# Kernel tuning notes

Hardware: AMD Instinct MI355X
Metric: run time of the kernel (lower is better)

The kernel has to match this reference:

```python
import jax, jax.numpy as jnp
import numpy as np

VOCAB = 50257
SMALL = 512
LARGE = 1024
B, S = 4, 2048


def setup_inputs() -> dict:
    key = jax.random.key(0)
    k1, k2, k3, k4 = jax.random.split(key, 4)
    input_ids = jax.random.randint(k1, (B, S), 0, VOCAB)
    weight = jax.random.normal(k2, (VOCAB, SMALL), dtype=jnp.float32) * 0.02
    # coeffs_weight stored as (large-small, small); init like normalized uniform
    cw = jax.random.uniform(k3, (LARGE - SMALL, SMALL), dtype=jnp.float32)
    coeffs_weight = cw / jnp.sum(cw, axis=-1, keepdims=True)
    residual_weight = jax.random.uniform(k4, (VOCAB, LARGE), dtype=jnp.float32,
                                         minval=-0.01, maxval=0.01)
    return {"input_ids": input_ids, "weight": weight,
            "coeffs_weight": coeffs_weight, "residual_weight": residual_weight}


def reference(input_ids, weight, coeffs_weight, residual_weight):
    # get_params(): expand width then add residual over the FULL vocab
    # expanded part: weight @ coeffs_weight.T -> (vocab, large-small)
    expanded = jnp.matmul(weight, coeffs_weight.T)
    full = jnp.concatenate([weight, expanded], axis=1) + residual_weight  # (vocab, large)
    # F.embedding gather
    return jnp.take(full, input_ids, axis=0)  # (B, S, large)
```

## Files before the change

### kernel.cpp

```cpp
#include <hip/hip_runtime.h>
#include <hip/hip_bf16.h>

typedef __attribute__((ext_vector_type(8))) short bf16x8;
typedef __attribute__((ext_vector_type(4))) float f32x4;

constexpr int VOCAB = 50257;
constexpr int SMALL = 512;
constexpr int LARGE = 1024;
constexpr int NTOK  = 4 * 2048;

static __device__ __forceinline__ unsigned short f2bf(float f) {
    __hip_bfloat16 h = __float2bfloat16(f);
    return *reinterpret_cast<unsigned short*>(&h);
}

__global__ __launch_bounds__(256) void k_gather(const int* __restrict__ ids,
                                                const float* __restrict__ weight,
                                                const float* __restrict__ residual,
                                                float* __restrict__ out,
                                                unsigned short* __restrict__ a_bf16) {
    int i  = blockIdx.x * 256 + threadIdx.x;
    int t  = i >> 7;
    int c  = (i & 127) << 2;
    int id = ids[t];
    const float4 w = *reinterpret_cast<const float4*>(weight   + (size_t)id * SMALL + c);
    const float4 r = *reinterpret_cast<const float4*>(residual + (size_t)id * LARGE + c);
    float4 o;
    o.x = w.x + r.x; o.y = w.y + r.y; o.z = w.z + r.z; o.w = w.w + r.w;
    *reinterpret_cast<float4*>(out + (size_t)t * LARGE + c) = o;
    ushort4 a;
    a.x = f2bf(w.x); a.y = f2bf(w.y); a.z = f2bf(w.z); a.w = f2bf(w.w);
    *reinterpret_cast<ushort4*>(a_bf16 + (size_t)t * SMALL + c) = a;
}

__global__ __launch_bounds__(256) void k_cvt_coeffs(const float* __restrict__ coeffs,
                                                    unsigned short* __restrict__ b_bf16) {
    int i = blockIdx.x * 256 + threadIdx.x;
    int e = i << 2;
    const float4 cvec = *reinterpret_cast<const float4*>(coeffs + e);
    ushort4 b;
    b.x = f2bf(cvec.x); b.y = f2bf(cvec.y); b.z = f2bf(cvec.z); b.w = f2bf(cvec.w);
    *reinterpret_cast<ushort4*>(b_bf16 + e) = b;
}

__global__ __launch_bounds__(256) void k_gemm(const int* __restrict__ ids,
                                              const unsigned short* __restrict__ A,
                                              const unsigned short* __restrict__ B,
                                              const float* __restrict__ residual,
                                              float* __restrict__ out) {
    const int wid  = threadIdx.x >> 6;
    const int lane = threadIdx.x & 63;
    const int bm   = blockIdx.x >> 3;
    const int bn   = blockIdx.x & 7;
    const int row0 = bm * 128 + wid * 32;
    const int col0 = bn * 64;
    const int lr   = lane & 15;
    const int lk   = (lane >> 4) * 8;

    f32x4 acc[2][4] = {};

    const unsigned short* pa0 = A + (size_t)(row0 + lr) * SMALL + lk;
    const unsigned short* pa1 = A + (size_t)(row0 + 16 + lr) * SMALL + lk;
    const unsigned short* pb  = B + (size_t)(col0 + lr) * SMALL + lk;

    for (int k0 = 0; k0 < 512; k0 += 32) {
        bf16x8 a0 = *reinterpret_cast<const bf16x8*>(pa0 + k0);
        bf16x8 a1 = *reinterpret_cast<const bf16x8*>(pa1 + k0);
        bf16x8 b0 = *reinterpret_cast<const bf16x8*>(pb + k0);
        bf16x8 b1 = *reinterpret_cast<const bf16x8*>(pb + 16 * SMALL + k0);
        bf16x8 b2 = *reinterpret_cast<const bf16x8*>(pb + 32 * SMALL + k0);
        bf16x8 b3 = *reinterpret_cast<const bf16x8*>(pb + 48 * SMALL + k0);
        acc[0][0] = __builtin_amdgcn_mfma_f32_16x16x32_bf16(a0, b0, acc[0][0], 0, 0, 0);
        acc[0][1] = __builtin_amdgcn_mfma_f32_16x16x32_bf16(a0, b1, acc[0][1], 0, 0, 0);
        acc[0][2] = __builtin_amdgcn_mfma_f32_16x16x32_bf16(a0, b2, acc[0][2], 0, 0, 0);
        acc[0][3] = __builtin_amdgcn_mfma_f32_16x16x32_bf16(a0, b3, acc[0][3], 0, 0, 0);
        acc[1][0] = __builtin_amdgcn_mfma_f32_16x16x32_bf16(a1, b0, acc[1][0], 0, 0, 0);
        acc[1][1] = __builtin_amdgcn_mfma_f32_16x16x32_bf16(a1, b1, acc[1][1], 0, 0, 0);
        acc[1][2] = __builtin_amdgcn_mfma_f32_16x16x32_bf16(a1, b2, acc[1][2], 0, 0, 0);
        acc[1][3] = __builtin_amdgcn_mfma_f32_16x16x32_bf16(a1, b3, acc[1][3], 0, 0, 0);
    }

    const int rbase = row0 + (lane >> 4) * 4;
    const int cbase = SMALL + col0 + lr;
#pragma unroll
    for (int m = 0; m < 2; ++m) {
#pragma unroll
        for (int r = 0; r < 4; ++r) {
            const int row = rbase + m * 16 + r;
            const int id  = ids[row];
            const float* res = residual + (size_t)id * LARGE + cbase;
            float*       op  = out      + (size_t)row * LARGE + cbase;
#pragma unroll
            for (int n = 0; n < 4; ++n)
                op[n * 16] = acc[m][n][r] + res[n * 16];
        }
    }
}

extern "C" void kernel_launch(void* const* d_in, const int* in_sizes, int n_in,
                              void* d_out, int out_size, void* d_ws, size_t ws_size,
                              hipStream_t stream) {
    const int*   ids      = (const int*)d_in[0];
    const float* weight   = (const float*)d_in[1];
    const float* coeffs   = (const float*)d_in[2];
    const float* residual = (const float*)d_in[3];
    float*       out      = (float*)d_out;

    unsigned short* a_bf16 = (unsigned short*)d_ws;
    unsigned short* b_bf16 = (unsigned short*)((char*)d_ws + (size_t)NTOK * SMALL * 2);

    k_gather<<<(NTOK * 128) / 256, 256, 0, stream>>>(ids, weight, residual, out, a_bf16);
    k_cvt_coeffs<<<(512 * 128) / 256, 256, 0, stream>>>(coeffs, b_bf16);
    k_gemm<<<512, 256, 0, stream>>>(ids, a_bf16, b_bf16, residual, out);
}
```

Measured before the change: 328.1 us.

## Fuse gather and bf16 GEMM into one kernel with shared-memory A tile

Result: slower. 339.2 us (+3.4%).

```diff
diff --git a/kernel.cpp b/kernel.cpp
--- a/kernel.cpp
+++ b/kernel.cpp
@@ -4,33 +4,15 @@
 typedef __attribute__((ext_vector_type(8))) short bf16x8;
 typedef __attribute__((ext_vector_type(4))) float f32x4;
 
-constexpr int VOCAB = 50257;
 constexpr int SMALL = 512;
 constexpr int LARGE = 1024;
 constexpr int NTOK  = 4 * 2048;
+constexpr int TPB   = 32;
+constexpr int LDA   = SMALL + 8;
 
 static __device__ __forceinline__ unsigned short f2bf(float f) {
     __hip_bfloat16 h = __float2bfloat16(f);
     return *reinterpret_cast<unsigned short*>(&h);
-}
-
-__global__ __launch_bounds__(256) void k_gather(const int* __restrict__ ids,
-                                                const float* __restrict__ weight,
-                                                const float* __restrict__ residual,
-                                                float* __restrict__ out,
-                                                unsigned short* __restrict__ a_bf16) {
-    int i  = blockIdx.x * 256 + threadIdx.x;
-    int t  = i >> 7;
-    int c  = (i & 127) << 2;
-    int id = ids[t];
-    const float4 w = *reinterpret_cast<const float4*>(weight   + (size_t)id * SMALL + c);
-    const float4 r = *reinterpret_cast<const float4*>(residual + (size_t)id * LARGE + c);
-    float4 o;
-    o.x = w.x + r.x; o.y = w.y + r.y; o.z = w.z + r.z; o.w = w.w + r.w;
-    *reinterpret_cast<float4*>(out + (size_t)t * LARGE + c) = o;
-    ushort4 a;
-    a.x = f2bf(w.x); a.y = f2bf(w.y); a.z = f2bf(w.z); a.w = f2bf(w.w);
-    *reinterpret_cast<ushort4*>(a_bf16 + (size_t)t * SMALL + c) = a;
 }
 
 __global__ __launch_bounds__(256) void k_cvt_coeffs(const float* __restrict__ coeffs,
@@ -43,57 +25,72 @@
     *reinterpret_cast<ushort4*>(b_bf16 + e) = b;
 }
 
-__global__ __launch_bounds__(256) void k_gemm(const int* __restrict__ ids,
-                                              const unsigned short* __restrict__ A,
-                                              const unsigned short* __restrict__ B,
-                                              const float* __restrict__ residual,
-                                              float* __restrict__ out) {
-    const int wid  = threadIdx.x >> 6;
-    const int lane = threadIdx.x & 63;
-    const int bm   = blockIdx.x >> 3;
-    const int bn   = blockIdx.x & 7;
-    const int row0 = bm * 128 + wid * 32;
-    const int col0 = bn * 64;
+__global__ __launch_bounds__(512) void k_fused(const int* __restrict__ ids,
+                                               const float* __restrict__ weight,
+                                               const float* __restrict__ residual,
+                                               const unsigned short* __restrict__ B,
+                                               float* __restrict__ out) {
+    __shared__ unsigned short As[TPB * LDA];
+    __shared__ int s_ids[TPB];
+
+    const int tid  = threadIdx.x;
+    const int tok0 = blockIdx.x * TPB;
+
+    if (tid < TPB) s_ids[tid] = ids[tok0 + tid];
+    __syncthreads();
+
+    {
+        const int t  = tid & 31;
+        const int c0 = (tid >> 5) * 32;
+        const int id = s_ids[t];
+        const float* wrow = weight   + (size_t)id * SMALL + c0;
+        const float* rrow = residual + (size_t)id * LARGE + c0;
+        float*       orow = out + (size_t)(tok0 + t) * LARGE + c0;
+        unsigned short* arow = As + t * LDA + c0;
+#pragma unroll
+        for (int j = 0; j < 8; ++j) {
+            const float4 w = *reinterpret_cast<const float4*>(wrow + 4 * j);
+            const float4 r = *reinterpret_cast<const float4*>(rrow + 4 * j);
+            float4 o;
+            o.x = w.x + r.x; o.y = w.y + r.y; o.z = w.z + r.z; o.w = w.w + r.w;
+            *reinterpret_cast<float4*>(orow + 4 * j) = o;
+            ushort4 a;
+            a.x = f2bf(w.x); a.y = f2bf(w.y); a.z = f2bf(w.z); a.w = f2bf(w.w);
+            *reinterpret_cast<ushort4*>(arow + 4 * j) = a;
+        }
+    }
+    __syncthreads();
+
+    const int wv   = tid >> 6;
+    const int lane = tid & 63;
+    const int r0   = (wv & 1) * 16;
+    const int c0b  = (wv >> 1) * 128;
     const int lr   = lane & 15;
     const int lk   = (lane >> 4) * 8;
 
-    f32x4 acc[2][4] = {};
-
-    const unsigned short* pa0 = A + (size_t)(row0 + lr) * SMALL + lk;
-    const unsigned short* pa1 = A + (size_t)(row0 + 16 + lr) * SMALL + lk;
-    const unsigned short* pb  = B + (size_t)(col0 + lr) * SMALL + lk;
+    f32x4 acc[8] = {};
+    const unsigned short* a_addr = As + (r0 + lr) * LDA + lk;
+    const unsigned short* pb     = B + (size_t)(c0b + lr) * SMALL + lk;
 
     for (int k0 = 0; k0 < 512; k0 += 32) {
-        bf16x8 a0 = *reinterpret_cast<const bf16x8*>(pa0 + k0);
-        bf16x8 a1 = *reinterpret_cast<const bf16x8*>(pa1 + k0);
-        bf16x8 b0 = *reinterpret_cast<const bf16x8*>(pb + k0);
-        bf16x8 b1 = *reinterpret_cast<const bf16x8*>(pb + 16 * SMALL + k0);
-        bf16x8 b2 = *reinterpret_cast<const bf16x8*>(pb + 32 * SMALL + k0);
-        bf16x8 b3 = *reinterpret_cast<const bf16x8*>(pb + 48 * SMALL + k0);
-        acc[0][0] = __builtin_amdgcn_mfma_f32_16x16x32_bf16(a0, b0, acc[0][0], 0, 0, 0);
-        acc[0][1] = __builtin_amdgcn_mfma_f32_16x16x32_bf16(a0, b1, acc[0][1], 0, 0, 0);
-        acc[0][2] = __builtin_amdgcn_mfma_f32_16x16x32_bf16(a0, b2, acc[0][2], 0, 0, 0);
-        acc[0][3] = __builtin_amdgcn_mfma_f32_16x16x32_bf16(a0, b3, acc[0][3], 0, 0, 0);
-        acc[1][0] = __builtin_amdgcn_mfma_f32_16x16x32_bf16(a1, b0, acc[1][0], 0, 0, 0);
-        acc[1][1] = __builtin_amdgcn_mfma_f32_16x16x32_bf16(a1, b1, acc[1][1], 0, 0, 0);
-        acc[1][2] = __builtin_amdgcn_mfma_f32_16x16x32_bf16(a1, b2, acc[1][2], 0, 0, 0);
-        acc[1][3] = __builtin_amdgcn_mfma_f32_16x16x32_bf16(a1, b3, acc[1][3], 0, 0, 0);
+        const bf16x8 a = *reinterpret_cast<const bf16x8*>(a_addr + k0);
+#pragma unroll
+        for (int n = 0; n < 8; ++n) {
+            const bf16x8 b = *reinterpret_cast<const bf16x8*>(pb + (size_t)n * 16 * SMALL + k0);
+            acc[n] = __builtin_amdgcn_mfma_f32_16x16x32_bf16(a, b, acc[n], 0, 0, 0);
+        }
     }
 
-    const int rbase = row0 + (lane >> 4) * 4;
-    const int cbase = SMALL + col0 + lr;
+    const int rloc = r0 + (lane >> 4) * 4;
 #pragma unroll
-    for (int m = 0; m < 2; ++m) {
+    for (int r = 0; r < 4; ++r) {
+        const int trow = rloc + r;
+        const int id2  = s_ids[trow];
+        const float* res = residual + (size_t)id2 * LARGE + SMALL + c0b + lr;
+        float*       op  = out + (size_t)(tok0 + trow) * LARGE + SMALL + c0b + lr;
 #pragma unroll
-        for (int r = 0; r < 4; ++r) {
-            const int row = rbase + m * 16 + r;
-            const int id  = ids[row];
-            const float* res = residual + (size_t)id * LARGE + cbase;
-            float*       op  = out      + (size_t)row * LARGE + cbase;
-#pragma unroll
-            for (int n = 0; n < 4; ++n)
-                op[n * 16] = acc[m][n][r] + res[n * 16];
-        }
+        for (int n = 0; n < 8; ++n)
+            op[n * 16] = acc[n][r] + res[n * 16];
     }
 }
 
@@ -106,10 +103,8 @@
     const float* residual = (const float*)d_in[3];
     float*       out      = (float*)d_out;
 
-    unsigned short* a_bf16 = (unsigned short*)d_ws;
-    unsigned short* b_bf16 = (unsigned short*)((char*)d_ws + (size_t)NTOK * SMALL * 2);
+    unsigned short* b_bf16 = (unsigned short*)d_ws;
 
-    k_gather<<<(NTOK * 128) / 256, 256, 0, stream>>>(ids, weight, residual, out, a_bf16);
     k_cvt_coeffs<<<(512 * 128) / 256, 256, 0, stream>>>(coeffs, b_bf16);
-    k_gemm<<<512, 256, 0, stream>>>(ids, a_bf16, b_bf16, residual, out);
+    k_fused<<<NTOK / TPB, 512, 0, stream>>>(ids, weight, residual, b_bf16, out);
 }
```
